# Kernel tuning notes

Hardware: AMD Instinct MI355X
Metric: run time of the kernel (lower is better)

The kernel has to match this reference:

```python
import jax, jax.numpy as jnp
import numpy as np

TOP_RATIO = 0.7
MIN_PATCHES = 128
RANDOM_RATIO = 0.1


def setup_inputs() -> dict:
    key = jax.random.key(0)
    k1, k2, k3, k4 = jax.random.split(key, 4)
    B, N, D, H = 4, 16384, 512, 256
    features = jax.random.normal(k1, (B, N, D), dtype=jnp.float32)
    W_V = jax.random.normal(k2, (D, H), dtype=jnp.float32) * (1.0 / np.sqrt(D))
    W_U = jax.random.normal(k3, (D, H), dtype=jnp.float32) * (1.0 / np.sqrt(D))
    w_att = jax.random.normal(k4, (H,), dtype=jnp.float32) * (1.0 / np.sqrt(H))
    return {
        "features": features,
        "W_V": W_V, "b_V": jnp.zeros((H,), jnp.float32),
        "W_U": W_U, "b_U": jnp.zeros((H,), jnp.float32),
        "w_att": w_att, "b_att": jnp.zeros((), jnp.float32),
    }


def reference(features, W_V, b_V, W_U, b_U, w_att, b_att):
    B, N, D = features.shape
    # gated attention scoring (dropout disabled: eval mode)
    a_V = jnp.tanh(features @ W_V + b_V)              # (B, N, H)
    a_U = jax.nn.sigmoid(features @ W_U + b_U)        # (B, N, H)
    raw = (a_V * a_U) @ w_att + b_att                 # (B, N)
    attn = jax.nn.softmax(raw, axis=-1)               # (B, N)

    # static selection sizes
    k = min(max(int(N * TOP_RATIO), MIN_PATCHES), N)  # 11468
    n_rand = max(int(k * RANDOM_RATIO), 1)            # 1146
    n_top = k - n_rand                                # 10322

    # batched top-k (softmax is monotone in raw, same indices as torch.topk(attn))
    _, top_idx = jax.lax.top_k(attn, n_top)           # (B, n_top)

    # remaining = indices not in top_idx, ascending; fixed count N - n_top
    mask = jnp.ones((B, N), bool).at[jnp.arange(B)[:, None], top_idx].set(False)
    remaining = jnp.argsort(~mask, axis=-1, stable=True)[:, : N - n_top]  # (B, N-n_top)

    # uniform random sample of n_rand remaining indices per batch element
    scores = jax.random.uniform(jax.random.key(42), (B, N - n_top))
    perm = jnp.argsort(scores, axis=-1)[:, :n_rand]   # random n_rand positions
    rand_idx = jnp.take_along_axis(remaining, perm, axis=-1)  # (B, n_rand)

    sel_idx = jnp.sort(jnp.concatenate([top_idx, rand_idx], axis=-1), axis=-1)  # (B, k)
    selected = jnp.take_along_axis(features, sel_idx[:, :, None], axis=1)       # (B, k, D)
    return selected, attn, sel_idx
```

## Files before the change

### kernel.cpp

```cpp
#include <hip/hip_runtime.h>
#include <stdint.h>

#define B 4
#define N 16384
#define D 512
#define H 256
#define NROWS (B * N)
#define K_SEL 11468
#define N_TOP 10322
#define N_RAND 1146
#define N_REM (N - N_TOP)
#define HALF_CNT ((B * N_REM) / 2)

typedef float f32x4 __attribute__((ext_vector_type(4)));
typedef _Float16 f16x8 __attribute__((ext_vector_type(8)));
typedef int i32x4 __attribute__((ext_vector_type(4)));

#define GLDS16(g, l)                                                    \
  __builtin_amdgcn_global_load_lds(                                     \
      (const __attribute__((address_space(1))) void*)(const void*)(g),  \
      (__attribute__((address_space(3))) void*)(void*)(l), 16, 0, 0)

__device__ __forceinline__ uint32_t f2key(float x) {
  uint32_t u = __float_as_uint(x);
  return u ^ ((u & 0x80000000u) ? 0xFFFFFFFFu : 0x80000000u);
}

__device__ __forceinline__ void threefry(uint32_t x0, uint32_t x1,
                                         uint32_t& o0, uint32_t& o1) {
  const uint32_t k0 = 0u, k1 = 42u;
  const uint32_t ks[3] = {k0, k1, k0 ^ k1 ^ 0x1BD11BDAu};
  x0 += ks[0];
  x1 += ks[1];
  const int R0[4] = {13, 15, 26, 6}, R1[4] = {17, 29, 16, 24};
#pragma unroll
  for (int i = 0; i < 5; ++i) {
    const int* R = (i & 1) ? R1 : R0;
#pragma unroll
    for (int jr = 0; jr < 4; ++jr) {
      x0 += x1;
      x1 = (x1 << R[jr]) | (x1 >> (32 - R[jr]));
      x1 ^= x0;
    }
    x0 += ks[(i + 1) % 3];
    x1 += ks[(i + 2) % 3] + (uint32_t)(i + 1);
  }
  o0 = x0;
  o1 = x1;
}

__device__ __forceinline__ void rand_body(const int b, int* __restrict__ psel,
                                          char* smem, const int t) {
  uint32_t* skey = reinterpret_cast<uint32_t*>(smem);
  uint32_t* hist = reinterpret_cast<uint32_t*>(smem + 24248);
  int* wr4 = reinterpret_cast<int*>(smem + 25272);
  uint32_t* shp = reinterpret_cast<uint32_t*>(smem + 25288);
  int* shrk = reinterpret_cast<int*>(smem + 25292);
  const int lane = t & 63, w4 = t >> 6;

  for (int p = t; p < N_REM; p += 256) {
    psel[b * N_REM + p] = 0;
    const int f = b * N_REM + p;
    uint32_t o0, o1, bits;
    if (f < HALF_CNT) {
      threefry((uint32_t)f, (uint32_t)(f + HALF_CNT), o0, o1);
      bits = o0;
    } else {
      threefry((uint32_t)(f - HALF_CNT), (uint32_t)f, o0, o1);
      bits = o1;
    }
    const float u = __uint_as_float((bits >> 9) | 0x3f800000u) - 1.0f;
    skey[p] = f2key(u);
  }
  __syncthreads();

  uint32_t prefix = 0;
  int rk = N_RAND;
  for (int pass = 3; pass >= 0; --pass) {
    const int sh = pass * 8;
    hist[t] = 0;
    __syncthreads();
    for (int p = t; p < N_REM; p += 256) {
      const uint32_t key = skey[p];
      if (pass == 3 || (key >> (sh + 8)) == (prefix >> (sh + 8)))
        atomicAdd(&hist[(key >> sh) & 255], 1u);
    }
    __syncthreads();
    const int h = (int)hist[t];
    int v = h;
#pragma unroll
    for (int off = 1; off < 64; off <<= 1) {
      const int u2 = __shfl_up(v, off, 64);
      if (lane >= off) v += u2;
    }
    if (lane == 63) wr4[w4] = v;
    __syncthreads();
    int add = 0;
    for (int i = 0; i < w4; ++i) add += wr4[i];
    const int incl = v + add, excl = incl - h;
    if (incl >= rk && excl < rk) {
      *shp = prefix | ((uint32_t)t << sh);
      *shrk = rk - excl;
    }
    __syncthreads();
    prefix = *shp;
    rk = *shrk;
    __syncthreads();
  }

  const int CH = 24;
  const int p0 = t * CH;
  const int pe = (p0 + CH < N_REM) ? p0 + CH : N_REM;
  int ce = 0;
  for (int p = p0; p < pe; ++p) ce += (skey[p] == prefix);
  int v = ce;
#pragma unroll
  for (int off = 1; off < 64; off <<= 1) {
    const int u2 = __shfl_up(v, off, 64);
    if (lane >= off) v += u2;
  }
  if (lane == 63) wr4[w4] = v;
  __syncthreads();
  if (t == 0) {
    int run = 0;
    for (int i = 0; i < 4; ++i) {
      const int a = wr4[i];
      wr4[i] = run;
      run += a;
    }
  }
  __syncthreads();
  int ge = wr4[w4] + v - ce;
  for (int p = p0; p < pe; ++p) {
    const uint32_t key = skey[p];
    const bool pick = (key < prefix) || (key == prefix && ge < rk);
    ge += (key == prefix);
    if (pick) psel[b * N_REM + p] = 1;
  }
}

__global__ __launch_bounds__(256) void prep_kernel(
    const float* __restrict__ WV, const float* __restrict__ WU,
    _Float16* __restrict__ wt_h, _Float16* __restrict__ wt_l,
    int* __restrict__ psel) {
  __shared__ __align__(16) char pmem[25296];
  if (blockIdx.x >= 64) {
    rand_body(blockIdx.x - 64, psel, pmem, threadIdx.x);
    return;
  }
  _Float16(*th)[65] = reinterpret_cast<_Float16(*)[65]>(pmem);
  _Float16(*tl)[65] = reinterpret_cast<_Float16(*)[65]>(pmem + 8320);
  const int kb = (blockIdx.x >> 3) * 64;
  const int nb = (blockIdx.x & 7) * 64;
  const int tx = threadIdx.x & 63;
  const int ty = threadIdx.x >> 6;
  const float* src = (nb < 256) ? WV : WU;
  const int nsrc = nb & 255;
#pragma unroll
  for (int i = 0; i < 16; ++i) {
    const int k = ty + i * 4;
    const float x = src[(size_t)(kb + k) * H + nsrc + tx];
    const _Float16 h = (_Float16)x;
    th[k][tx] = h;
    tl[k][tx] = (_Float16)(x - (float)h);
  }
  __syncthreads();
  const int n_local = threadIdx.x & 63;
  const int c2 = threadIdx.x >> 6;
  const int s_local = c2 >> 1, half = c2 & 1;
  const int n = nb + n_local;
  const int s = (kb >> 5) + s_local;
  const int klb = s_local * 32 + half * 16;
  f16x8 vh0, vh1, vl0, vl1;
#pragma unroll
  for (int e = 0; e < 8; ++e) {
    vh0[e] = th[klb + e][n_local];
    vh1[e] = th[klb + 8 + e][n_local];
    vl0[e] = tl[klb + e][n_local];
    vl1[e] = tl[klb + 8 + e][n_local];
  }
  const size_t o = (size_t)s * 16384 + (size_t)n * 32 + half * 16;
  *reinterpret_cast<f16x8*>(wt_h + o) = vh0;
  *reinterpret_cast<f16x8*>(wt_h + o + 8) = vh1;
  *reinterpret_cast<f16x8*>(wt_l + o) = vl0;
  *reinterpret_cast<f16x8*>(wt_l + o + 8) = vl1;
}

__global__ __launch_bounds__(512) void score_kernel(
    const float* __restrict__ feat, const _Float16* __restrict__ wt_h,
    const _Float16* __restrict__ wt_l, const float* __restrict__ bV,
    const float* __restrict__ bU, const float* __restrict__ watt,
    float* __restrict__ raw) {
  __shared__ _Float16 Ah[128 * 32];
  __shared__ _Float16 Al[128 * 32];
  __shared__ _Float16 Bh0[512 * 32];
  __shared__ _Float16 Bl0[512 * 32];
  __shared__ _Float16 Bh1[512 * 32];
  __shared__ _Float16 Bl1[512 * 32];
  __shared__ float red[128][5];

  const int tid = threadIdx.x;
  const int lane = tid & 63;
  const int lc = lane & 15;
  const int lg = lane >> 4;
  const int w = __builtin_amdgcn_readfirstlane(tid >> 6);
  const int rg = w >> 2;
  const int cg = w & 3;
  const int row0 = blockIdx.x * 128;

  const int rA = tid >> 2;
  const int gA = tid & 3;
  const float* aG = feat + (size_t)(row0 + rA) * D + gA * 8;
  const int awOff = rA * 32 + gA * 8;

  const _Float16* pbh = wt_h + (size_t)w * 2048 + lane * 8;
  const _Float16* pbl = wt_l + (size_t)w * 2048 + lane * 8;
  const int ldsB = w * 2048;

  int aoff[4], boff[8];
#pragma unroll
  for (int mt = 0; mt < 4; ++mt)
    aoff[mt] = (rg * 64 + mt * 16 + lc) * 32 + lg * 8;
#pragma unroll
  for (int nt = 0; nt < 8; ++nt) {
    const int nbase =
        (nt < 4) ? cg * 64 + nt * 16 : 256 + cg * 64 + (nt - 4) * 16;
    boff[nt] = (nbase + lc) * 32 + lg * 8;
  }

  f32x4 acc[4][8] = {};
  f32x4 a0, a1;

  a0 = *(const f32x4*)(aG);
  a1 = *(const f32x4*)(aG + 4);
#pragma unroll
  for (int i = 0; i < 4; ++i) {
    GLDS16(pbh + i * 512, &Bh0[ldsB + i * 512]);
    GLDS16(pbl + i * 512, &Bl0[ldsB + i * 512]);
  }
  {
    f16x8 ahw, alw;
#pragma unroll
    for (int e = 0; e < 8; ++e) {
      const float x = (e < 4) ? a0[e] : a1[e - 4];
      const _Float16 h = (_Float16)x;
      ahw[e] = h;
      alw[e] = (_Float16)(x - (float)h);
    }
    *(f16x8*)&Ah[awOff] = ahw;
    *(f16x8*)&Al[awOff] = alw;
  }
  __syncthreads();

#pragma unroll 1
  for (int kt = 0; kt < 16; ++kt) {
    const int knx = (kt + 1) & 15;
    _Float16* BhN = (kt & 1) ? Bh0 : Bh1;
    _Float16* BlN = (kt & 1) ? Bl0 : Bl1;
    const _Float16* BhC = (kt & 1) ? Bh1 : Bh0;
    const _Float16* BlC = (kt & 1) ? Bl1 : Bl0;

#pragma unroll
    for (int i = 0; i < 4; ++i) {
      GLDS16(pbh + knx * 16384 + i * 512, &BhN[ldsB + i * 512]);
      GLDS16(pbl + knx * 16384 + i * 512, &BlN[ldsB + i * 512]);
    }
    a0 = *(const f32x4*)(aG + knx * 32);
    a1 = *(const f32x4*)(aG + knx * 32 + 4);
    __builtin_amdgcn_sched_barrier(0);

    f16x8 ah[4], al[4];
#pragma unroll
    for (int mt = 0; mt < 4; ++mt) {
      ah[mt] = *(const f16x8*)&Ah[aoff[mt]];
      al[mt] = *(const f16x8*)&Al[aoff[mt]];
    }
#pragma unroll
    for (int nt = 0; nt < 8; ++nt) {
      const f16x8 bh = *(const f16x8*)&BhC[boff[nt]];
      const f16x8 bl = *(const f16x8*)&BlC[boff[nt]];
#pragma unroll
      for (int mt = 0; mt < 4; ++mt) {
        acc[mt][nt] = __builtin_amdgcn_mfma_f32_16x16x32_f16(ah[mt], bh,
                                                             acc[mt][nt], 0, 0, 0);
        acc[mt][nt] = __builtin_amdgcn_mfma_f32_16x16x32_f16(ah[mt], bl,
                                                             acc[mt][nt], 0, 0, 0);
        acc[mt][nt] = __builtin_amdgcn_mfma_f32_16x16x32_f16(al[mt], bh,
                                                             acc[mt][nt], 0, 0, 0);
      }
    }
    __syncthreads();

    {
      f16x8 ahw, alw;
#pragma unroll
      for (int e = 0; e < 8; ++e) {
        const float x = (e < 4) ? a0[e] : a1[e - 4];
        const _Float16 h = (_Float16)x;
        ahw[e] = h;
        alw[e] = (_Float16)(x - (float)h);
      }
      *(f16x8*)&Ah[awOff] = ahw;
      *(f16x8*)&Al[awOff] = alw;
    }
    __syncthreads();
  }

#pragma unroll
  for (int mt = 0; mt < 4; ++mt) {
    float rs[4] = {0.f, 0.f, 0.f, 0.f};
#pragma unroll
    for (int nt = 0; nt < 4; ++nt) {
      const int j = cg * 64 + nt * 16 + lc;
      const float bv = bV[j], bu = bU[j], wa = watt[j];
#pragma unroll
      for (int rr = 0; rr < 4; ++rr) {
        const float cV = acc[mt][nt][rr] + bv;
        const float cU = acc[mt][nt + 4][rr] + bu;
        const float e2 = __expf(2.0f * cV);
        const float aV = 1.0f - 2.0f / (e2 + 1.0f);
        const float aU = 1.0f / (1.0f + __expf(-cU));
        rs[rr] += aV * aU * wa;
      }
    }
#pragma unroll
    for (int rr = 0; rr < 4; ++rr) {
      float v = rs[rr];
      v += __shfl_xor(v, 1, 16);
      v += __shfl_xor(v, 2, 16);
      v += __shfl_xor(v, 4, 16);
      v += __shfl_xor(v, 8, 16);
      if (lc == 0) red[rg * 64 + mt * 16 + lg * 4 + rr][cg] = v;
    }
  }
  __syncthreads();
  if (tid < 128)
    raw[row0 + tid] = red[tid][0] + red[tid][1] + red[tid][2] + red[tid][3];
}

__device__ __forceinline__ int scan1024(int c, int* wred, int tid) {
  const int lane = tid & 63, w = tid >> 6;
  int v = c;
#pragma unroll
  for (int off = 1; off < 64; off <<= 1) {
    const int u = __shfl_up(v, off, 64);
    if (lane >= off) v += u;
  }
  if (lane == 63) wred[w] = v;
  __syncthreads();
  if (tid == 0) {
    int run = 0;
    for (int i = 0; i < 16; ++i) {
      const int a = wred[i];
      wred[i] = run;
      run += a;
    }
  }
  __syncthreads();
  const int res = wred[w] + v - c;
  __syncthreads();
  return res;
}

__global__ __launch_bounds__(1024) void select_kernel(
    const float* __restrict__ raw, const int* __restrict__ psel,
    float* __restrict__ attn_out, int* __restrict__ sel_ws,
    float* __restrict__ out_selidx) {
  const int b = blockIdx.x, t = threadIdx.x;
  const int lane = t & 63, w = t >> 6;
  __shared__ float sraw[N];
  __shared__ int whist[16][256];
  __shared__ int ghist[256];
  __shared__ float fred[16];
  __shared__ int wred[16];
  __shared__ float shM, shS;
  __shared__ uint32_t sh_prefix;
  __shared__ int sh_rk;
  const float* r = raw + b * N;

  float m = -3.0e38f;
  for (int i = 0; i < 16; ++i) {
    const int idx = t + i * 1024;
    const float v = r[idx];
    sraw[idx] = v;
    m = fmaxf(m, v);
  }
  for (int off = 32; off > 0; off >>= 1) m = fmaxf(m, __shfl_down(m, off, 64));
  if (lane == 0) fred[w] = m;
  __syncthreads();
  if (t == 0) {
    float mm = fred[0];
    for (int i = 1; i < 16; ++i) mm = fmaxf(mm, fred[i]);
    shM = mm;
  }
  __syncthreads();
  const float M = shM;

  float ex[16];
  float s = 0.f;
  for (int i = 0; i < 16; ++i) {
    ex[i] = expf(sraw[t + i * 1024] - M);
    s += ex[i];
  }
  for (int off = 32; off > 0; off >>= 1) s += __shfl_down(s, off, 64);
  if (lane == 0) fred[w] = s;
  __syncthreads();
  if (t == 0) {
    float ss = 0.f;
    for (int i = 0; i < 16; ++i) ss += fred[i];
    shS = ss;
  }
  __syncthreads();
  const float inv = 1.0f / shS;

  for (int i = 0; i < 16; ++i)
    attn_out[b * N + t + i * 1024] = ex[i] * inv;

  uint32_t prefix = 0;
  int rk = N_TOP;
  for (int pass = 3; pass >= 0; --pass) {
    const int sh = pass * 8;
#pragma unroll
    for (int q = 0; q < 4; ++q) whist[w][lane * 4 + q] = 0;
    __syncthreads();
    for (int i = 0; i < 16; ++i) {
      const uint32_t key = f2key(sraw[t + i * 1024]);
      if (pass == 3 || (key >> (sh + 8)) == (prefix >> (sh + 8)))
        atomicAdd(&whist[w][(key >> sh) & 255], 1);
    }
    __syncthreads();
    if (t < 256) {
      int tot = 0;
      for (int ww = 0; ww < 16; ++ww) tot += whist[ww][t];
      ghist[t] = tot;
    }
    __syncthreads();
    int vS = 0, hrev = 0;
    if (t < 256) {
      hrev = ghist[255 - t];
      vS = hrev;
#pragma unroll
      for (int off = 1; off < 64; off <<= 1) {
        const int u2 = __shfl_up(vS, off, 64);
        if (lane >= off) vS += u2;
      }
      if (lane == 63) wred[t >> 6] = vS;
    }
    __syncthreads();
    if (t < 256) {
      int add = 0;
      const int w4 = t >> 6;
      for (int i = 0; i < w4; ++i) add += wred[i];
      const int incl = vS + add, excl = incl - hrev;
      if (incl >= rk && excl < rk) {
        sh_prefix = prefix | ((uint32_t)(255 - t) << sh);
        sh_rk = rk - excl;
      }
    }
    __syncthreads();
    prefix = sh_prefix;
    rk = sh_rk;
    __syncthreads();
  }
  const uint32_t T = prefix;
  const int tieTake = rk;

  const int n0 = t * 16;
  int cgt = 0, ceq = 0;
  for (int i = 0; i < 16; ++i) {
    const uint32_t key = f2key(sraw[n0 + i]);
    cgt += (key > T);
    ceq += (key == T);
  }
  const int gbase = scan1024(cgt, wred, t);
  const int ebase = scan1024(ceq, wred, t);
  int grun = gbase, erun = ebase;
  unsigned selmask = 0;
  int csel = 0;
  for (int i = 0; i < 16; ++i) {
    const int n = n0 + i;
    const uint32_t key = f2key(sraw[n]);
    const bool gt = key > T, eq = key == T;
    const bool mem = gt || (eq && erun < tieTake);
    int sel;
    if (mem) {
      sel = 1;
    } else {
      const int members_before = grun + (erun < tieTake ? erun : tieTake);
      const int p = n - members_before;
      sel = psel[b * N_REM + p];
    }
    selmask |= (unsigned)sel << i;
    csel += sel;
    grun += gt;
    erun += eq;
  }
  int q = scan1024(csel, wred, t);
  for (int i = 0; i < 16; ++i) {
    if ((selmask >> i) & 1) {
      const int n = n0 + i;
      sel_ws[b * K_SEL + q] = n;
      out_selidx[b * K_SEL + q] = (float)n;
      ++q;
    }
  }
}

__global__ __launch_bounds__(128) void gather_kernel(
    const float* __restrict__ feat, const int* __restrict__ sel_ws,
    float* __restrict__ out_sel) {
  const int qa = blockIdx.x;
  const int b = qa / K_SEL;
  const int n = sel_ws[qa];
  const float4* src =
      reinterpret_cast<const float4*>(feat + (size_t)(b * N + n) * D);
  float4* dst = reinterpret_cast<float4*>(out_sel + (size_t)qa * D);
  dst[threadIdx.x] = src[threadIdx.x];
}

extern "C" void kernel_launch(void* const* d_in, const int* in_sizes, int n_in,
                              void* d_out, int out_size, void* d_ws,
                              size_t ws_size, hipStream_t stream) {
  const float* feat = (const float*)d_in[0];
  const float* WV = (const float*)d_in[1];
  const float* bV = (const float*)d_in[2];
  const float* WU = (const float*)d_in[3];
  const float* bU = (const float*)d_in[4];
  const float* watt = (const float*)d_in[5];
  const float* batt = (const float*)d_in[6];
  (void)batt;

  float* out = (float*)d_out;
  float* out_selected = out;
  float* out_attn = out + (size_t)B * K_SEL * D;
  float* out_selidx = out_attn + (size_t)B * N;

  _Float16* wt_h = (_Float16*)d_ws;
  _Float16* wt_l = wt_h + 512 * 512;
  float* raw = (float*)(wt_l + 512 * 512);
  int* psel = (int*)(raw + NROWS);
  int* sel_ws = psel + B * N_REM;

  prep_kernel<<<68, 256, 0, stream>>>(WV, WU, wt_h, wt_l, psel);
  score_kernel<<<NROWS / 128, 512, 0, stream>>>(feat, wt_h, wt_l, bV, bU, watt,
                                                raw);
  select_kernel<<<B, 1024, 0, stream>>>(raw, psel, out_attn, sel_ws,
                                        out_selidx);
  gather_kernel<<<B * K_SEL, 128, 0, stream>>>(feat, sel_ws, out_selected);
}
```

Before: 351.3 us.

## Swizzle LDS layouts for A and B tiles and software-pipeline B fragment loads

Applies an XOR swizzle on the 8-element column groups of both the repacked weight layout and the A tile in LDS, so MFMA fragment reads avoid bank conflicts. The B fragment loads in the inner MFMA loop are double-buffered in registers so the next tile's load overlaps the current MFMAs. The loop raises wave priority around the MFMA block and moves the fp16 split of the next A chunk before the barrier. This costs extra index arithmetic and register pressure, and the prep and consumer kernels must agree on the swizzle.

```diff
diff --git a/kernel.cpp b/kernel.cpp
--- a/kernel.cpp
+++ b/kernel.cpp
@@ -171,6 +171,7 @@
   const int n = nb + n_local;
   const int s = (kb >> 5) + s_local;
   const int klb = s_local * 32 + half * 16;
+  const int swz = (n_local >> 1) & 3;
   f16x8 vh0, vh1, vl0, vl1;
 #pragma unroll
   for (int e = 0; e < 8; ++e) {
@@ -179,11 +180,11 @@
     vl0[e] = tl[klb + e][n_local];
     vl1[e] = tl[klb + 8 + e][n_local];
   }
-  const size_t o = (size_t)s * 16384 + (size_t)n * 32 + half * 16;
-  *reinterpret_cast<f16x8*>(wt_h + o) = vh0;
-  *reinterpret_cast<f16x8*>(wt_h + o + 8) = vh1;
-  *reinterpret_cast<f16x8*>(wt_l + o) = vl0;
-  *reinterpret_cast<f16x8*>(wt_l + o + 8) = vl1;
+  const size_t orow = (size_t)s * 16384 + (size_t)n * 32;
+  *reinterpret_cast<f16x8*>(wt_h + orow + (((2 * half) ^ swz) * 8)) = vh0;
+  *reinterpret_cast<f16x8*>(wt_h + orow + (((2 * half + 1) ^ swz) * 8)) = vh1;
+  *reinterpret_cast<f16x8*>(wt_l + orow + (((2 * half) ^ swz) * 8)) = vl0;
+  *reinterpret_cast<f16x8*>(wt_l + orow + (((2 * half + 1) ^ swz) * 8)) = vl1;
 }
 
 __global__ __launch_bounds__(512) void score_kernel(
@@ -211,21 +212,22 @@
   const int rA = tid >> 2;
   const int gA = tid & 3;
   const float* aG = feat + (size_t)(row0 + rA) * D + gA * 8;
-  const int awOff = rA * 32 + gA * 8;
+  const int awOff = rA * 32 + ((gA ^ ((rA >> 1) & 3)) << 3);
 
   const _Float16* pbh = wt_h + (size_t)w * 2048 + lane * 8;
   const _Float16* pbl = wt_l + (size_t)w * 2048 + lane * 8;
   const int ldsB = w * 2048;
 
+  const int rswz = (lc >> 1) & 3;
   int aoff[4], boff[8];
 #pragma unroll
   for (int mt = 0; mt < 4; ++mt)
-    aoff[mt] = (rg * 64 + mt * 16 + lc) * 32 + lg * 8;
+    aoff[mt] = (rg * 64 + mt * 16 + lc) * 32 + ((lg ^ rswz) << 3);
 #pragma unroll
   for (int nt = 0; nt < 8; ++nt) {
     const int nbase =
         (nt < 4) ? cg * 64 + nt * 16 : 256 + cg * 64 + (nt - 4) * 16;
-    boff[nt] = (nbase + lc) * 32 + lg * 8;
+    boff[nt] = (nbase + lc) * 32 + ((lg ^ rswz) << 3);
   }
 
   f32x4 acc[4][8] = {};
@@ -275,10 +277,16 @@
       ah[mt] = *(const f16x8*)&Ah[aoff[mt]];
       al[mt] = *(const f16x8*)&Al[aoff[mt]];
     }
+    f16x8 bh = *(const f16x8*)&BhC[boff[0]];
+    f16x8 bl = *(const f16x8*)&BlC[boff[0]];
+    __builtin_amdgcn_s_setprio(1);
 #pragma unroll
     for (int nt = 0; nt < 8; ++nt) {
-      const f16x8 bh = *(const f16x8*)&BhC[boff[nt]];
-      const f16x8 bl = *(const f16x8*)&BlC[boff[nt]];
+      f16x8 bhn, bln;
+      if (nt < 7) {
+        bhn = *(const f16x8*)&BhC[boff[nt + 1]];
+        bln = *(const f16x8*)&BlC[boff[nt + 1]];
+      }
 #pragma unroll
       for (int mt = 0; mt < 4; ++mt) {
         acc[mt][nt] = __builtin_amdgcn_mfma_f32_16x16x32_f16(ah[mt], bh,
@@ -288,21 +296,22 @@
         acc[mt][nt] = __builtin_amdgcn_mfma_f32_16x16x32_f16(al[mt], bh,
                                                              acc[mt][nt], 0, 0, 0);
       }
-    }
-    __syncthreads();
-
-    {
-      f16x8 ahw, alw;
-#pragma unroll
-      for (int e = 0; e < 8; ++e) {
-        const float x = (e < 4) ? a0[e] : a1[e - 4];
-        const _Float16 h = (_Float16)x;
-        ahw[e] = h;
-        alw[e] = (_Float16)(x - (float)h);
-      }
-      *(f16x8*)&Ah[awOff] = ahw;
-      *(f16x8*)&Al[awOff] = alw;
-    }
+      bh = bhn;
+      bl = bln;
+    }
+    __builtin_amdgcn_s_setprio(0);
+
+    f16x8 ahw, alw;
+#pragma unroll
+    for (int e = 0; e < 8; ++e) {
+      const float x = (e < 4) ? a0[e] : a1[e - 4];
+      const _Float16 h = (_Float16)x;
+      ahw[e] = h;
+      alw[e] = (_Float16)(x - (float)h);
+    }
+    __syncthreads();
+    *(f16x8*)&Ah[awOff] = ahw;
+    *(f16x8*)&Al[awOff] = alw;
     __syncthreads();
   }
 
```

Result: no change. 351.4 us (+0.0%).
